# Kernel optimization log

Hardware: AMD Instinct MI355X
Metric: run time of the kernel (lower is better)

The kernel has to match this reference:

```python
import jax, jax.numpy as jnp
import numpy as np

TOP_K = 2

def moe_linear(x, router_w, experts_w):
    # x: [T, din]; router_w: [din, E]; experts_w: [E, din, dout]
    T = x.shape[0]
    E = experts_w.shape[0]
    probs = jax.nn.softmax(x @ router_w, axis=-1)            # [T, E]
    topv, topi = jax.lax.top_k(probs, TOP_K)                 # [T, k]
    topv = topv / jnp.sum(topv, axis=-1, keepdims=True)      # renormalize over selected experts
    w = jnp.zeros((T, E), x.dtype).at[jnp.arange(T)[:, None], topi].set(topv)  # dense routing weights
    y = jnp.zeros((T, experts_w.shape[2]), x.dtype)
    for e in range(E):  # small fixed expert loop; avoids [T,E,dout] intermediate
        y = y + w[:, e:e+1] * (x @ experts_w[e])
    return y

def setup_inputs() -> dict:
    key = jax.random.key(0)
    ks = jax.random.split(key, 7)
    B, S, H, I, E = 4, 2048, 1024, 3584, 8
    sH, sI = 1.0 / np.sqrt(H), 1.0 / np.sqrt(I)
    return {
        "hidden_state": jax.random.normal(ks[0], (B, S, H), jnp.float32),
        "gate_router": jax.random.normal(ks[1], (H, E), jnp.float32) * sH,
        "gate_experts": jax.random.normal(ks[2], (E, H, I), jnp.float32) * sH,
        "up_router": jax.random.normal(ks[3], (H, E), jnp.float32) * sH,
        "up_experts": jax.random.normal(ks[4], (E, H, I), jnp.float32) * sH,
        "down_router": jax.random.normal(ks[5], (I, E), jnp.float32) * sI,
        "down_experts": jax.random.normal(ks[6], (E, I, H), jnp.float32) * sI,
    }

def reference(hidden_state, gate_router, gate_experts, up_router, up_experts, down_router, down_experts):
    B, S, H = hidden_state.shape
    x = hidden_state.reshape(B * S, H)
    g = moe_linear(x, gate_router, gate_experts)             # [T, I]
    u = moe_linear(x, up_router, up_experts)                 # [T, I]
    h = jax.nn.silu(g) * u                                   # SwiGLU
    y = moe_linear(h, down_router, down_experts)             # [T, H]
    return y.reshape(B, S, H)
```

## Files before the change

### kernel.cpp

```cpp
#include <hip/hip_runtime.h>
#include <stdint.h>
#include <stdio.h>

#define T_TOK 8192
#define HDIM  1024
#define IDIM  3584
#define NEXP  8
#define NPAIR (T_TOK*2)
#define BM 128
#define BN 128
#define BK 32

typedef float          f32x4 __attribute__((ext_vector_type(4)));
typedef short          s16x8 __attribute__((ext_vector_type(8)));
typedef unsigned short u16x4 __attribute__((ext_vector_type(4)));
typedef unsigned short u16x8 __attribute__((ext_vector_type(8)));

__device__ __forceinline__ unsigned short f2bf_rne(float f) {
  unsigned u = __float_as_uint(f);
  u += 0x7FFFu + ((u >> 16) & 1u);
  return (unsigned short)(u >> 16);
}
__device__ __forceinline__ float bf2f(unsigned short h) {
  return __uint_as_float(((unsigned)h) << 16);
}

__device__ __forceinline__ void gld16(const void* gsrc, void* ldst) {
  typedef const unsigned int __attribute__((address_space(1))) GU;
  typedef unsigned int       __attribute__((address_space(3))) LU;
  __builtin_amdgcn_global_load_lds((GU*)(unsigned long long)gsrc,
                                   (LU*)(unsigned int)(unsigned long long)ldst,
                                   16, 0, 0);
}

__global__ void split_hilo(const float* __restrict__ in,
                           unsigned short* __restrict__ hi,
                           unsigned short* __restrict__ lo, int n4) {
  int i = blockIdx.x*blockDim.x + threadIdx.x;
  int s = gridDim.x*blockDim.x;
  for (; i < n4; i += s) {
    f32x4 v = ((const f32x4*)in)[i];
    u16x4 h, l;
#pragma unroll
    for (int j = 0; j < 4; j++) {
      float f = v[j];
      unsigned short hb = f2bf_rne(f);
      h[j] = hb;
      l[j] = f2bf_rne(f - bf2f(hb));
    }
    ((u16x4*)hi)[i] = h;
    ((u16x4*)lo)[i] = l;
  }
}

__global__ void transpose_split(const float* __restrict__ W,
                                unsigned short* __restrict__ hi,
                                unsigned short* __restrict__ lo,
                                int K, int N) {
  __shared__ float tile[32][33];
  long base = (long)blockIdx.z * K * N;
  int n0 = blockIdx.x*32, k0 = blockIdx.y*32;
  int tx = threadIdx.x, ty = threadIdx.y;
#pragma unroll
  for (int r = 0; r < 4; r++)
    tile[ty+8*r][tx] = W[base + (long)(k0+ty+8*r)*N + n0 + tx];
  __syncthreads();
#pragma unroll
  for (int r = 0; r < 4; r++) {
    float f = tile[tx][ty+8*r];
    long o = base + (long)(n0+ty+8*r)*K + k0 + tx;
    unsigned short hb = f2bf_rne(f);
    hi[o] = hb;
    if (lo) lo[o] = f2bf_rne(f - bf2f(hb));
  }
}

__device__ __forceinline__ void top2_write(const float* acc, int t,
                                           int* __restrict__ topi,
                                           float* __restrict__ topw) {
  int i0 = 0; float l0 = acc[0];
#pragma unroll
  for (int e = 1; e < NEXP; e++) if (acc[e] > l0) { l0 = acc[e]; i0 = e; }
  int i1 = -1; float l1 = -3.4e38f;
#pragma unroll
  for (int e = 0; e < NEXP; e++) if (e != i0 && acc[e] > l1) { l1 = acc[e]; i1 = e; }
  float w0 = 1.f/(1.f + expf(l1 - l0));
  float w1 = 1.f/(1.f + expf(l0 - l1));
  topi[2*t]   = i0; topi[2*t+1] = i1;
  topw[2*t]   = w0; topw[2*t+1] = w1;
}

__global__ __launch_bounds__(256) void router2_topk(
    const float* __restrict__ X,
    const float* __restrict__ RWg, const float* __restrict__ RWu,
    int* __restrict__ tig, float* __restrict__ twg,
    int* __restrict__ tiu, float* __restrict__ twu) {
  int lane = threadIdx.x & 63;
  int t = blockIdx.x*4 + (threadIdx.x>>6);
  const f32x4* xr = (const f32x4*)(X + (long)t*HDIM);
  float ag[NEXP], au[NEXP];
#pragma unroll
  for (int e = 0; e < NEXP; e++) { ag[e] = 0.f; au[e] = 0.f; }
#pragma unroll
  for (int it = 0; it < HDIM/4/64; it++) {
    int c4 = it*64 + lane;
    f32x4 xv = xr[c4];
#pragma unroll
    for (int j = 0; j < 4; j++) {
      const float* wg = RWg + (long)(c4*4+j)*NEXP;
      const float* wu = RWu + (long)(c4*4+j)*NEXP;
#pragma unroll
      for (int e = 0; e < NEXP; e++) { ag[e] += xv[j]*wg[e]; au[e] += xv[j]*wu[e]; }
    }
  }
#pragma unroll
  for (int e = 0; e < NEXP; e++) {
    float vg = ag[e], vu = au[e];
#pragma unroll
    for (int o = 1; o < 64; o <<= 1) { vg += __shfl_xor(vg, o); vu += __shfl_xor(vu, o); }
    ag[e] = vg; au[e] = vu;
  }
  if (lane == 0) { top2_write(ag, t, tig, twg); top2_write(au, t, tiu, twu); }
}

__global__ __launch_bounds__(256) void build_perm(const int* __restrict__ topi,
                                                  const float* __restrict__ topw,
                                                  int* __restrict__ offs,
                                                  int* __restrict__ ptok,
                                                  float* __restrict__ pw) {
  int e = blockIdx.x;
  int tid = threadIdx.x, lane = tid & 63, wv = tid >> 6;
  __shared__ int cnt[NEXP];
  __shared__ int wsum[4];
  if (tid < NEXP) cnt[tid] = 0;
  __syncthreads();
  for (int p = tid; p < NPAIR; p += 256) atomicAdd(&cnt[topi[p]], 1);
  __syncthreads();
  int base = 0;
#pragma unroll
  for (int e2 = 0; e2 < NEXP; e2++) if (e2 < e) base += cnt[e2];
  if (tid == 0) { offs[e] = base; if (e == NEXP-1) offs[NEXP] = base + cnt[e]; }
  for (int p0 = 0; p0 < NPAIR; p0 += 256) {
    int p = p0 + tid;
    bool m = (topi[p] == e);
    unsigned long long b = __ballot(m);
    int lp = __popcll(b & ((1ull << lane) - 1ull));
    if (lane == 0) wsum[wv] = __popcll(b);
    __syncthreads();
    int woff = 0;
#pragma unroll
    for (int w2 = 0; w2 < 4; w2++) if (w2 < wv) woff += wsum[w2];
    int tot = wsum[0] + wsum[1] + wsum[2] + wsum[3];
    if (m) { int dst = base + woff + lp; ptok[dst] = p >> 1; pw[dst] = topw[p]; }
    base += tot;
    __syncthreads();
  }
}

__global__ __launch_bounds__(256) void moe_gemm3(
    const unsigned short* __restrict__ Ahi, const unsigned short* __restrict__ Alo,
    const unsigned short* __restrict__ Bhi, const unsigned short* __restrict__ Blo,
    const int* __restrict__ offs, const int* __restrict__ ptok,
    const float* __restrict__ pw, float* __restrict__ out, int K, int N)
{
  const int e = blockIdx.z;
  const int beg = offs[e];
  const int cnt = offs[e+1] - beg;
  const int m0 = blockIdx.y * BM;
  if (m0 >= cnt) return;
  const int n0 = blockIdx.x * BN;

  __shared__ unsigned short Ah[BM*BK], Al[BM*BK], Bh[BN*BK], Bl[BN*BK];
  __shared__ int   stok[BM];
  __shared__ float swt[BM];

  const int tid = threadIdx.x, lane = tid & 63, wv = tid >> 6;
  if (tid < BM) {
    int i = m0 + tid;
    stok[tid] = ptok[beg + (i < cnt ? i : 0)];
    swt[tid]  = (i < cnt) ? pw[beg + i] : 0.f;
  }
  __syncthreads();

  const int srow = lane >> 2;
  const int scol = (lane & 3) * 8;
  const int r0 = (wv*2+0)*16 + srow;
  const int r1 = (wv*2+1)*16 + srow;
  const long a0 = (long)stok[r0]*K + scol;
  const long a1 = (long)stok[r1]*K + scol;
  const long b0 = ((long)e*N + n0 + r0)*K + scol;
  const long b1 = ((long)e*N + n0 + r1)*K + scol;
  unsigned short* dA0  = &Ah[(wv*2+0)*16*BK];
  unsigned short* dA1  = &Ah[(wv*2+1)*16*BK];
  unsigned short* dAl0 = &Al[(wv*2+0)*16*BK];
  unsigned short* dAl1 = &Al[(wv*2+1)*16*BK];
  unsigned short* dB0  = &Bh[(wv*2+0)*16*BK];
  unsigned short* dB1  = &Bh[(wv*2+1)*16*BK];
  unsigned short* dBl0 = &Bl[(wv*2+0)*16*BK];
  unsigned short* dBl1 = &Bl[(wv*2+1)*16*BK];

  f32x4 zero = {0.f, 0.f, 0.f, 0.f};
  f32x4 acc[4][4];
#pragma unroll
  for (int i = 0; i < 4; i++)
#pragma unroll
    for (int j = 0; j < 4; j++) acc[i][j] = zero;

  const int arow = (wv>>1)*64, bcol = (wv&1)*64;
  const int fl = lane & 15, fg = lane >> 4;

  for (int kk = 0; kk < K; kk += BK) {
    __syncthreads();
    gld16(Ahi + a0 + kk, dA0);  gld16(Ahi + a1 + kk, dA1);
    gld16(Alo + a0 + kk, dAl0); gld16(Alo + a1 + kk, dAl1);
    gld16(Bhi + b0 + kk, dB0);  gld16(Bhi + b1 + kk, dB1);
    gld16(Blo + b0 + kk, dBl0); gld16(Blo + b1 + kk, dBl1);
    asm volatile("s_waitcnt vmcnt(0)" ::: "memory");
    __syncthreads();

    s16x8 ahf[4], alf[4], bhf[4], blf[4];
#pragma unroll
    for (int i = 0; i < 4; i++) {
      ahf[i] = *(const s16x8*)&Ah[(arow + i*16 + fl)*BK + fg*8];
      alf[i] = *(const s16x8*)&Al[(arow + i*16 + fl)*BK + fg*8];
      bhf[i] = *(const s16x8*)&Bh[(bcol + i*16 + fl)*BK + fg*8];
      blf[i] = *(const s16x8*)&Bl[(bcol + i*16 + fl)*BK + fg*8];
    }
#pragma unroll
    for (int i = 0; i < 4; i++)
#pragma unroll
      for (int j = 0; j < 4; j++) {
        acc[i][j] = __builtin_amdgcn_mfma_f32_16x16x32_bf16(ahf[i], bhf[j], acc[i][j], 0,0,0);
        acc[i][j] = __builtin_amdgcn_mfma_f32_16x16x32_bf16(alf[i], bhf[j], acc[i][j], 0,0,0);
        acc[i][j] = __builtin_amdgcn_mfma_f32_16x16x32_bf16(ahf[i], blf[j], acc[i][j], 0,0,0);
      }
  }

#pragma unroll
  for (int i = 0; i < 4; i++)
#pragma unroll
    for (int r = 0; r < 4; r++) {
      int lrow = arow + i*16 + fg*4 + r;
      if (m0 + lrow < cnt) {
        float wt = swt[lrow];
        long ob = (long)stok[lrow]*N + n0 + bcol + fl;
#pragma unroll
        for (int j = 0; j < 4; j++)
          atomicAdd(&out[ob + j*16], wt * acc[i][j][r]);
      }
    }
}

__global__ __launch_bounds__(256) void swiglu_router(
    float* __restrict__ g, const float* __restrict__ u,
    const float* __restrict__ RW,
    int* __restrict__ topi, float* __restrict__ topw) {
  int lane = threadIdx.x & 63;
  int t = blockIdx.x*4 + (threadIdx.x>>6);
  f32x4*       gr = (f32x4*)(g + (long)t*IDIM);
  const f32x4* ur = (const f32x4*)(u + (long)t*IDIM);
  float acc[NEXP];
#pragma unroll
  for (int e = 0; e < NEXP; e++) acc[e] = 0.f;
#pragma unroll
  for (int it = 0; it < IDIM/4/64; it++) {
    int c4 = it*64 + lane;
    f32x4 gv = gr[c4], uv = ur[c4], hv;
#pragma unroll
    for (int j = 0; j < 4; j++) {
      float x = gv[j];
      hv[j] = x * uv[j] / (1.f + expf(-x));
    }
    gr[c4] = hv;
#pragma unroll
    for (int j = 0; j < 4; j++) {
      const float* wr = RW + (long)(c4*4+j)*NEXP;
#pragma unroll
      for (int e = 0; e < NEXP; e++) acc[e] += hv[j]*wr[e];
    }
  }
#pragma unroll
  for (int e = 0; e < NEXP; e++) {
    float v = acc[e];
#pragma unroll
    for (int o = 1; o < 64; o <<= 1) v += __shfl_xor(v, o);
    acc[e] = v;
  }
  if (lane == 0) top2_write(acc, t, topi, topw);
}

__global__ __launch_bounds__(256) void moe_gemm_down(
    const float* __restrict__ Hf, const unsigned short* __restrict__ Bw,
    const int* __restrict__ offs, const int* __restrict__ ptok,
    const float* __restrict__ pw, float* __restrict__ out)
{
  const int K = IDIM, N = HDIM;
  const int e = blockIdx.z;
  const int beg = offs[e];
  const int cnt = offs[e+1] - beg;
  const int m0 = blockIdx.y * BM;
  if (m0 >= cnt) return;
  const int n0 = blockIdx.x * BN;

  __shared__ unsigned short Ah[BM*BK], Bh[BN*BK];
  __shared__ int   stok[BM];
  __shared__ float swt[BM];

  const int tid = threadIdx.x, lane = tid & 63, wv = tid >> 6;
  if (tid < BM) {
    int i = m0 + tid;
    stok[tid] = ptok[beg + (i < cnt ? i : 0)];
    swt[tid]  = (i < cnt) ? pw[beg + i] : 0.f;
  }
  __syncthreads();

  const int arw = tid >> 1, half = tid & 1;
  const float* asrc = Hf + (long)stok[arw]*K + half*16;
  const int awoff = arw*BK + half*16;

  const int srow = lane >> 2, scol = (lane & 3)*8;
  const int r0 = (wv*2+0)*16 + srow, r1 = (wv*2+1)*16 + srow;
  const long b0 = ((long)e*N + n0 + r0)*K + scol;
  const long b1 = ((long)e*N + n0 + r1)*K + scol;
  unsigned short* dB0 = &Bh[(wv*2+0)*16*BK];
  unsigned short* dB1 = &Bh[(wv*2+1)*16*BK];

  f32x4 zero = {0.f,0.f,0.f,0.f};
  f32x4 acc[4][4];
#pragma unroll
  for (int i = 0; i < 4; i++)
#pragma unroll
    for (int j = 0; j < 4; j++) acc[i][j] = zero;

  const int arow = (wv>>1)*64, bcol = (wv&1)*64;
  const int fl = lane & 15, fg = lane >> 4;

  f32x4 p0, p1, p2, p3;
#define LOADA(kk) do {                        \
    p0 = ((const f32x4*)(asrc + (kk)))[0];    \
    p1 = ((const f32x4*)(asrc + (kk)))[1];    \
    p2 = ((const f32x4*)(asrc + (kk)))[2];    \
    p3 = ((const f32x4*)(asrc + (kk)))[3];    \
  } while (0)

  LOADA(0);

  for (int kk = 0; kk < K; kk += BK) {
    __syncthreads();
    gld16(Bw + b0 + kk, dB0);
    gld16(Bw + b1 + kk, dB1);
    u16x8 ha, hb2;
    ha[0]=f2bf_rne(p0[0]); ha[1]=f2bf_rne(p0[1]); ha[2]=f2bf_rne(p0[2]); ha[3]=f2bf_rne(p0[3]);
    ha[4]=f2bf_rne(p1[0]); ha[5]=f2bf_rne(p1[1]); ha[6]=f2bf_rne(p1[2]); ha[7]=f2bf_rne(p1[3]);
    hb2[0]=f2bf_rne(p2[0]); hb2[1]=f2bf_rne(p2[1]); hb2[2]=f2bf_rne(p2[2]); hb2[3]=f2bf_rne(p2[3]);
    hb2[4]=f2bf_rne(p3[0]); hb2[5]=f2bf_rne(p3[1]); hb2[6]=f2bf_rne(p3[2]); hb2[7]=f2bf_rne(p3[3]);
    *(u16x8*)&Ah[awoff]   = ha;
    *(u16x8*)&Ah[awoff+8] = hb2;
    asm volatile("s_waitcnt vmcnt(0)" ::: "memory");
    __syncthreads();

    if (kk + BK < K) LOADA(kk + BK);

    s16x8 ahf[4], bhf[4];
#pragma unroll
    for (int i = 0; i < 4; i++) {
      ahf[i] = *(const s16x8*)&Ah[(arow + i*16 + fl)*BK + fg*8];
      bhf[i] = *(const s16x8*)&Bh[(bcol + i*16 + fl)*BK + fg*8];
    }
#pragma unroll
    for (int i = 0; i < 4; i++)
#pragma unroll
      for (int j = 0; j < 4; j++)
        acc[i][j] = __builtin_amdgcn_mfma_f32_16x16x32_bf16(ahf[i], bhf[j], acc[i][j], 0,0,0);
  }
#undef LOADA

#pragma unroll
  for (int i = 0; i < 4; i++)
#pragma unroll
    for (int r = 0; r < 4; r++) {
      int lrow = arow + i*16 + fg*4 + r;
      if (m0 + lrow < cnt) {
        float wt = swt[lrow];
        long ob = (long)stok[lrow]*N + n0 + bcol + fl;
#pragma unroll
        for (int j = 0; j < 4; j++)
          atomicAdd(&out[ob + j*16], wt * acc[i][j][r]);
      }
    }
}

extern "C" void kernel_launch(void* const* d_in, const int* in_sizes, int n_in,
                              void* d_out, int out_size, void* d_ws, size_t ws_size,
                              hipStream_t stream)
{
  (void)in_sizes; (void)n_in;
  const float* x   = (const float*)d_in[0];
  const float* grt = (const float*)d_in[1];
  const float* gex = (const float*)d_in[2];
  const float* urt = (const float*)d_in[3];
  const float* uex = (const float*)d_in[4];
  const float* drt = (const float*)d_in[5];
  const float* dex = (const float*)d_in[6];
  float* out = (float*)d_out;

  char* base = (char*)d_ws;
  size_t off = 0;
  auto alloc = [&](size_t b) -> void* {
    void* r = base + off;
    off = (off + b + 255) & ~(size_t)255;
    return r;
  };
  const size_t szXH = (size_t)T_TOK*HDIM*2;
  const size_t szW  = (size_t)NEXP*HDIM*IDIM*2;
  const size_t szGI = (size_t)T_TOK*IDIM*4;

  unsigned short* xhi   = (unsigned short*)alloc(szXH);
  unsigned short* xlo   = (unsigned short*)alloc(szXH);
  unsigned short* wg_hi = (unsigned short*)alloc(szW);
  unsigned short* wg_lo = (unsigned short*)alloc(szW);
  unsigned short* wu_hi = (unsigned short*)alloc(szW);
  unsigned short* wu_lo = (unsigned short*)alloc(szW);
  float* gbuf = (float*)alloc(szGI);
  int*   topi_g = (int*)alloc(NPAIR*4);  float* topw_g = (float*)alloc(NPAIR*4);
  int*   topi_u = (int*)alloc(NPAIR*4);  float* topw_u = (float*)alloc(NPAIR*4);
  int*   topi_d = (int*)alloc(NPAIR*4);  float* topw_d = (float*)alloc(NPAIR*4);
  int* offs_g = (int*)alloc(64);
  int* offs_u = (int*)alloc(64);
  int* offs_d = (int*)alloc(64);
  int*   ptok_g = (int*)alloc(NPAIR*4);  float* pw_g = (float*)alloc(NPAIR*4);
  int*   ptok_u = (int*)alloc(NPAIR*4);  float* pw_u = (float*)alloc(NPAIR*4);
  int*   ptok_d = (int*)alloc(NPAIR*4);  float* pw_d = (float*)alloc(NPAIR*4);

  float*          ubuf  = (float*)wg_hi;
  unsigned short* wd_hi = wu_hi;

  if (off > ws_size) {
    fprintf(stderr, "[moe] ws too small: need %zu bytes, have %zu\n", off, ws_size);
    hipMemsetAsync(d_out, 0, (size_t)out_size*sizeof(float), stream);
    return;
  }

  hipMemsetAsync(gbuf, 0, szGI, stream);
  hipMemsetAsync(d_out, 0, (size_t)out_size*sizeof(float), stream);

  split_hilo<<<2048, 256, 0, stream>>>(x, xhi, xlo, T_TOK*HDIM/4);
  transpose_split<<<dim3(IDIM/32, HDIM/32, NEXP), dim3(32,8), 0, stream>>>(gex, wg_hi, wg_lo, HDIM, IDIM);
  transpose_split<<<dim3(IDIM/32, HDIM/32, NEXP), dim3(32,8), 0, stream>>>(uex, wu_hi, wu_lo, HDIM, IDIM);
  router2_topk<<<T_TOK/4, 256, 0, stream>>>(x, grt, urt, topi_g, topw_g, topi_u, topw_u);
  build_perm<<<NEXP, 256, 0, stream>>>(topi_g, topw_g, offs_g, ptok_g, pw_g);
  build_perm<<<NEXP, 256, 0, stream>>>(topi_u, topw_u, offs_u, ptok_u, pw_u);

  moe_gemm3<<<dim3(IDIM/BN, T_TOK/BM, NEXP), 256, 0, stream>>>(
      xhi, xlo, wg_hi, wg_lo, offs_g, ptok_g, pw_g, gbuf, HDIM, IDIM);

  hipMemsetAsync(ubuf, 0, szGI, stream);
  moe_gemm3<<<dim3(IDIM/BN, T_TOK/BM, NEXP), 256, 0, stream>>>(
      xhi, xlo, wu_hi, wu_lo, offs_u, ptok_u, pw_u, ubuf, HDIM, IDIM);

  transpose_split<<<dim3(HDIM/32, IDIM/32, NEXP), dim3(32,8), 0, stream>>>(dex, wd_hi, nullptr, IDIM, HDIM);

  swiglu_router<<<T_TOK/4, 256, 0, stream>>>(gbuf, ubuf, drt, topi_d, topw_d);
  build_perm<<<NEXP, 256, 0, stream>>>(topi_d, topw_d, offs_d, ptok_d, pw_d);

  moe_gemm_down<<<dim3(HDIM/BN, T_TOK/BM, NEXP), 256, 0, stream>>>(
      gbuf, wd_hi, offs_d, ptok_d, pw_d, out);
}
```

Before: 1.781 ms.

## Rewrite gate/up MoE GEMM with 256x256 tiles and triple-buffered LDS prefetch

Replaces the 128x128, 4-wave gate/up expert GEMM with a 256x256, 8-wave kernel. The three split-precision products (hi·hi, lo·hi, hi·lo) become a single flattened 96-step K loop. Loads go into a triple-buffered, swizzled LDS ring and are issued two steps ahead with partial vmcnt waits and MFMA priority raising. The goal is to overlap global loads with MFMA work, remove the per-step full drain, and raise operand reuse per tile. In exchange it uses much more LDS and registers, which limits occupancy, and the larger M tile wastes more work on sparsely filled expert tiles.

```diff
diff --git a/kernel.cpp b/kernel.cpp
--- a/kernel.cpp
+++ b/kernel.cpp
@@ -10,6 +10,7 @@
 #define BM 128
 #define BN 128
 #define BK 32
+#define NTK  96
 
 typedef float          f32x4 __attribute__((ext_vector_type(4)));
 typedef short          s16x8 __attribute__((ext_vector_type(8)));
@@ -157,25 +158,26 @@
   }
 }
 
-__global__ __launch_bounds__(256) void moe_gemm3(
+__global__ __launch_bounds__(512, 2) void moe_gemm3_8p(
     const unsigned short* __restrict__ Ahi, const unsigned short* __restrict__ Alo,
     const unsigned short* __restrict__ Bhi, const unsigned short* __restrict__ Blo,
     const int* __restrict__ offs, const int* __restrict__ ptok,
-    const float* __restrict__ pw, float* __restrict__ out, int K, int N)
+    const float* __restrict__ pw, float* __restrict__ out)
 {
   const int e = blockIdx.z;
   const int beg = offs[e];
   const int cnt = offs[e+1] - beg;
-  const int m0 = blockIdx.y * BM;
+  const int m0 = blockIdx.y * 256;
   if (m0 >= cnt) return;
-  const int n0 = blockIdx.x * BN;
-
-  __shared__ unsigned short Ah[BM*BK], Al[BM*BK], Bh[BN*BK], Bl[BN*BK];
-  __shared__ int   stok[BM];
-  __shared__ float swt[BM];
+  const int n0 = blockIdx.x * 256;
+
+  __shared__ unsigned short AsL[3][256*32];
+  __shared__ unsigned short BsL[3][256*32];
+  __shared__ int   stok[256];
+  __shared__ float swt[256];
 
   const int tid = threadIdx.x, lane = tid & 63, wv = tid >> 6;
-  if (tid < BM) {
+  if (tid < 256) {
     int i = m0 + tid;
     stok[tid] = ptok[beg + (i < cnt ? i : 0)];
     swt[tid]  = (i < cnt) ? pw[beg + i] : 0.f;
@@ -183,70 +185,98 @@
   __syncthreads();
 
   const int srow = lane >> 2;
-  const int scol = (lane & 3) * 8;
-  const int r0 = (wv*2+0)*16 + srow;
-  const int r1 = (wv*2+1)*16 + srow;
-  const long a0 = (long)stok[r0]*K + scol;
-  const long a1 = (long)stok[r1]*K + scol;
-  const long b0 = ((long)e*N + n0 + r0)*K + scol;
-  const long b1 = ((long)e*N + n0 + r1)*K + scol;
-  unsigned short* dA0  = &Ah[(wv*2+0)*16*BK];
-  unsigned short* dA1  = &Ah[(wv*2+1)*16*BK];
-  unsigned short* dAl0 = &Al[(wv*2+0)*16*BK];
-  unsigned short* dAl1 = &Al[(wv*2+1)*16*BK];
-  unsigned short* dB0  = &Bh[(wv*2+0)*16*BK];
-  unsigned short* dB1  = &Bh[(wv*2+1)*16*BK];
-  unsigned short* dBl0 = &Bl[(wv*2+0)*16*BK];
-  unsigned short* dBl1 = &Bl[(wv*2+1)*16*BK];
-
-  f32x4 zero = {0.f, 0.f, 0.f, 0.f};
-  f32x4 acc[4][4];
-#pragma unroll
-  for (int i = 0; i < 4; i++)
-#pragma unroll
-    for (int j = 0; j < 4; j++) acc[i][j] = zero;
-
-  const int arow = (wv>>1)*64, bcol = (wv&1)*64;
+  const int lc   = ((lane & 3) - ((lane >> 3) & 3)) & 3;
+  const long aoff0 = (long)stok[wv*32 +      srow]*HDIM + lc*8;
+  const long aoff1 = (long)stok[wv*32 + 16 + srow]*HDIM + lc*8;
+  const long boff0 = ((long)e*IDIM + n0 + wv*32 +      srow)*HDIM + lc*8;
+  const long boff1 = ((long)e*IDIM + n0 + wv*32 + 16 + srow)*HDIM + lc*8;
+  const int adst0 = (wv*32     )*32;
+  const int adst1 = (wv*32 + 16)*32;
+
+#define STAGE_A(buf, kt) do {                                              \
+    int s_ = (kt) >> 5; int kl_ = ((kt) & 31) * 32;                        \
+    const unsigned short* ap_ = (s_ == 1) ? Alo : Ahi;                     \
+    gld16(ap_ + aoff0 + kl_, &AsL[buf][adst0]);                            \
+    gld16(ap_ + aoff1 + kl_, &AsL[buf][adst1]);                            \
+  } while (0)
+#define STAGE_B(buf, kt) do {                                              \
+    int s_ = (kt) >> 5; int kl_ = ((kt) & 31) * 32;                        \
+    const unsigned short* bp_ = (s_ == 2) ? Blo : Bhi;                     \
+    gld16(bp_ + boff0 + kl_, &BsL[buf][adst0]);                            \
+    gld16(bp_ + boff1 + kl_, &BsL[buf][adst1]);                            \
+  } while (0)
+
   const int fl = lane & 15, fg = lane >> 4;
-
-  for (int kk = 0; kk < K; kk += BK) {
-    __syncthreads();
-    gld16(Ahi + a0 + kk, dA0);  gld16(Ahi + a1 + kk, dA1);
-    gld16(Alo + a0 + kk, dAl0); gld16(Alo + a1 + kk, dAl1);
-    gld16(Bhi + b0 + kk, dB0);  gld16(Bhi + b1 + kk, dB1);
-    gld16(Blo + b0 + kk, dBl0); gld16(Blo + b1 + kk, dBl1);
-    asm volatile("s_waitcnt vmcnt(0)" ::: "memory");
-    __syncthreads();
-
-    s16x8 ahf[4], alf[4], bhf[4], blf[4];
-#pragma unroll
-    for (int i = 0; i < 4; i++) {
-      ahf[i] = *(const s16x8*)&Ah[(arow + i*16 + fl)*BK + fg*8];
-      alf[i] = *(const s16x8*)&Al[(arow + i*16 + fl)*BK + fg*8];
-      bhf[i] = *(const s16x8*)&Bh[(bcol + i*16 + fl)*BK + fg*8];
-      blf[i] = *(const s16x8*)&Bl[(bcol + i*16 + fl)*BK + fg*8];
-    }
+  const int pks = (((fg + (fl >> 1)) & 3) << 3);
+  const int wm = wv >> 2, wn = wv & 3;
+  const int arow = wm * 128;
+  const int bcol = wn * 64;
+
+  f32x4 acc[8][4];
+#pragma unroll
+  for (int m = 0; m < 8; m++)
+#pragma unroll
+    for (int n = 0; n < 4; n++) acc[m][n] = {0.f, 0.f, 0.f, 0.f};
+
+  STAGE_A(0, 0); STAGE_B(0, 0);
+  STAGE_A(1, 1); STAGE_B(1, 1);
+  asm volatile("s_waitcnt vmcnt(0)" ::: "memory");
+  __syncthreads();
+
+  int buf = 0, nbuf = 2;
+  for (int kt = 0; kt < NTK; ++kt) {
+    const bool st = (kt + 2 < NTK);
+    s16x8 bhf[4], ahf[4];
+
+    if (st) STAGE_A(nbuf, kt + 2);
+#pragma unroll
+    for (int n = 0; n < 4; n++)
+      bhf[n] = *(const s16x8*)&BsL[buf][(bcol + n*16 + fl)*32 + pks];
 #pragma unroll
     for (int i = 0; i < 4; i++)
-#pragma unroll
-      for (int j = 0; j < 4; j++) {
-        acc[i][j] = __builtin_amdgcn_mfma_f32_16x16x32_bf16(ahf[i], bhf[j], acc[i][j], 0,0,0);
-        acc[i][j] = __builtin_amdgcn_mfma_f32_16x16x32_bf16(alf[i], bhf[j], acc[i][j], 0,0,0);
-        acc[i][j] = __builtin_amdgcn_mfma_f32_16x16x32_bf16(ahf[i], blf[j], acc[i][j], 0,0,0);
-      }
-  }
-
-#pragma unroll
-  for (int i = 0; i < 4; i++)
+      ahf[i] = *(const s16x8*)&AsL[buf][(arow + i*16 + fl)*32 + pks];
+    __builtin_amdgcn_s_setprio(1);
+#pragma unroll
+    for (int i = 0; i < 4; i++)
+#pragma unroll
+      for (int n = 0; n < 4; n++)
+        acc[i][n] = __builtin_amdgcn_mfma_f32_16x16x32_bf16(ahf[i], bhf[n], acc[i][n], 0,0,0);
+    __builtin_amdgcn_s_setprio(0);
+
+    if (st) STAGE_B(nbuf, kt + 2);
+#pragma unroll
+    for (int i = 0; i < 4; i++)
+      ahf[i] = *(const s16x8*)&AsL[buf][(arow + (4+i)*16 + fl)*32 + pks];
+    __builtin_amdgcn_s_setprio(1);
+#pragma unroll
+    for (int i = 0; i < 4; i++)
+#pragma unroll
+      for (int n = 0; n < 4; n++)
+        acc[4+i][n] = __builtin_amdgcn_mfma_f32_16x16x32_bf16(ahf[i], bhf[n], acc[4+i][n], 0,0,0);
+    __builtin_amdgcn_s_setprio(0);
+
+    if (st) asm volatile("s_waitcnt vmcnt(4)" ::: "memory");
+    else    asm volatile("s_waitcnt vmcnt(0)" ::: "memory");
+    __builtin_amdgcn_s_barrier();
+    __builtin_amdgcn_sched_barrier(0);
+
+    buf  = (buf  == 2) ? 0 : buf + 1;
+    nbuf = (nbuf == 2) ? 0 : nbuf + 1;
+  }
+#undef STAGE_A
+#undef STAGE_B
+
+#pragma unroll
+  for (int m = 0; m < 8; m++)
 #pragma unroll
     for (int r = 0; r < 4; r++) {
-      int lrow = arow + i*16 + fg*4 + r;
+      int lrow = arow + m*16 + fg*4 + r;
       if (m0 + lrow < cnt) {
         float wt = swt[lrow];
-        long ob = (long)stok[lrow]*N + n0 + bcol + fl;
-#pragma unroll
-        for (int j = 0; j < 4; j++)
-          atomicAdd(&out[ob + j*16], wt * acc[i][j][r]);
+        long ob = (long)stok[lrow]*IDIM + n0 + bcol + fl;
+#pragma unroll
+        for (int n = 0; n < 4; n++)
+          atomicAdd(&out[ob + n*16], wt * acc[m][n][r]);
       }
     }
 }
@@ -451,12 +481,12 @@
   build_perm<<<NEXP, 256, 0, stream>>>(topi_g, topw_g, offs_g, ptok_g, pw_g);
   build_perm<<<NEXP, 256, 0, stream>>>(topi_u, topw_u, offs_u, ptok_u, pw_u);
 
-  moe_gemm3<<<dim3(IDIM/BN, T_TOK/BM, NEXP), 256, 0, stream>>>(
-      xhi, xlo, wg_hi, wg_lo, offs_g, ptok_g, pw_g, gbuf, HDIM, IDIM);
+  moe_gemm3_8p<<<dim3(IDIM/256, 64, NEXP), 512, 0, stream>>>(
+      xhi, xlo, wg_hi, wg_lo, offs_g, ptok_g, pw_g, gbuf);
 
   hipMemsetAsync(ubuf, 0, szGI, stream);
-  moe_gemm3<<<dim3(IDIM/BN, T_TOK/BM, NEXP), 256, 0, stream>>>(
-      xhi, xlo, wu_hi, wu_lo, offs_u, ptok_u, pw_u, ubuf, HDIM, IDIM);
+  moe_gemm3_8p<<<dim3(IDIM/256, 64, NEXP), 512, 0, stream>>>(
+      xhi, xlo, wu_hi, wu_lo, offs_u, ptok_u, pw_u, ubuf);
 
   transpose_split<<<dim3(HDIM/32, IDIM/32, NEXP), dim3(32,8), 0, stream>>>(dex, wd_hi, nullptr, IDIM, HDIM);
 
```

After: 1.843 ms. 3.5% more time.
